# Optimization experiments

Hardware: AMD Instinct MI355X
Metric: run time of the kernel (lower is better)

The kernel has to match this reference:

```python
import jax, jax.numpy as jnp
import numpy as np
from jax import lax

B, T, CIN, H, W = 2, 6, 1, 256, 256
COUT = 64
L = 13
H2, W2 = H // 2, W // 2


def conv2d(x, w, b, stride=1, pad=0):
    y = lax.conv_general_dilated(x, w, (stride, stride), [(pad, pad), (pad, pad)],
                                 dimension_numbers=('NCHW', 'OIHW', 'NCHW'))
    return y + b[None, :, None, None]


def leaky(x):
    return jnp.where(x >= 0, x, 0.2 * x)


def bilinear_sample(img, sx, sy):
    # img [B,C,H,W]; sx,sy [B,L,H,W] pixel coords; zero padding (grid_sample align_corners=True)
    Bc, C, Hh, Ww = img.shape
    x0 = jnp.floor(sx); y0 = jnp.floor(sy)
    x1 = x0 + 1.0; y1 = y0 + 1.0
    wx1 = sx - x0; wx0 = 1.0 - wx1
    wy1 = sy - y0; wy0 = 1.0 - wy1
    img_flat = img.reshape(Bc, C, Hh * Ww)

    def gather(xi, yi):
        valid = (xi >= 0) & (xi <= Ww - 1) & (yi >= 0) & (yi <= Hh - 1)
        xc = jnp.clip(xi, 0, Ww - 1).astype(jnp.int32)
        yc = jnp.clip(yi, 0, Hh - 1).astype(jnp.int32)
        idx = (yc * Ww + xc).reshape(Bc, 1, -1)
        g = jnp.take_along_axis(img_flat, idx, axis=2).reshape(Bc, C, *xi.shape[1:])
        return g * valid[:, None].astype(img.dtype)  # [B,C,L,H,W]

    return (gather(x0, y0) * (wx0 * wy0)[:, None]
            + gather(x1, y0) * (wx1 * wy0)[:, None]
            + gather(x0, y1) * (wx0 * wy1)[:, None]
            + gather(x1, y1) * (wx1 * wy1)[:, None])


def setup_inputs() -> dict:
    key = jax.random.key(0)
    ks = jax.random.split(key, 14)
    s = 0.05
    return {
        'x': jax.random.normal(ks[0], (B, T, CIN, H, W), jnp.float32),
        'w_stem': jax.random.normal(ks[1], (COUT * T, CIN * T, 3, 3), jnp.float32) * s,
        'b_stem': jnp.zeros((COUT * T,), jnp.float32),
        'w_i2h': jax.random.normal(ks[2], (3 * COUT, COUT, 3, 3), jnp.float32) * s,
        'b_i2h': jnp.zeros((3 * COUT,), jnp.float32),
        'w_i2f': jax.random.normal(ks[3], (32, COUT, 5, 5), jnp.float32) * s,
        'b_i2f': jnp.zeros((32,), jnp.float32),
        'w_h2f': jax.random.normal(ks[4], (32, COUT, 5, 5), jnp.float32) * s,
        'b_h2f': jnp.zeros((32,), jnp.float32),
        'w_flow': jax.random.normal(ks[5], (L * 2, 32, 5, 5), jnp.float32) * s,
        'b_flow': jnp.zeros((L * 2,), jnp.float32),
        'w_ret': jax.random.normal(ks[6], (3 * COUT, L * COUT, 1, 1), jnp.float32) * s,
        'b_ret': jnp.zeros((3 * COUT,), jnp.float32),
    }


def reference(x, w_stem, b_stem, w_i2h, b_i2h, w_i2f, b_i2f, w_h2f, b_h2f,
              w_flow, b_flow, w_ret, b_ret):
    Bq, Tq, Cq, Hq, Wq = x.shape
    h2, w2 = Hq // 2, Wq // 2
    # stem: fold T into channels, strided conv + leaky relu
    xs = x.reshape(Bq, Tq * Cq, Hq, Wq)
    ys = leaky(conv2d(xs, w_stem, b_stem, stride=2, pad=1))
    ys = ys.reshape(Bq, Tq, COUT, h2, w2)
    seq = jnp.transpose(ys, (1, 0, 2, 3, 4))  # [T,B,C,h,w]

    gy, gx = jnp.meshgrid(jnp.arange(h2, dtype=jnp.float32),
                          jnp.arange(w2, dtype=jnp.float32), indexing='ij')

    def step(hprev, xt):
        i2h = conv2d(xt, w_i2h, b_i2h, pad=1)  # [B,3C,h,w]
        f1 = leaky(conv2d(xt, w_i2f, b_i2f, pad=2) + conv2d(hprev, w_h2f, b_h2f, pad=2))
        flows = conv2d(f1, w_flow, b_flow, pad=2).reshape(Bq, L, 2, h2, w2)
        u, v = flows[:, :, 0], flows[:, :, 1]
        # wrap(h, -flow): sample at grid - flow
        sx = gx[None, None] - u
        sy = gy[None, None] - v
        warped = bilinear_sample(hprev, sx, sy)  # [B,C,L,h,w]
        warped = jnp.transpose(warped, (0, 2, 1, 3, 4)).reshape(Bq, L * COUT, h2, w2)
        h2h = conv2d(warped, w_ret, b_ret)  # 1x1 conv
        ir, iu, im = jnp.split(i2h, 3, axis=1)
        hr, hu, hm = jnp.split(h2h, 3, axis=1)
        r = jax.nn.sigmoid(ir + hr)
        z = jax.nn.sigmoid(iu + hu)
        m = leaky(im + r * hm)
        hnext = z * hprev + (1.0 - z) * m
        return hnext, hnext

    h0 = jnp.zeros((Bq, COUT, h2, w2), x.dtype)
    _, outs = lax.scan(step, h0, seq)  # [T,B,C,h,w]
    return jnp.transpose(outs, (1, 0, 2, 3, 4))
```

## Files before the change

kernel.cpp:

```cpp
#include <hip/hip_runtime.h>
#include <cstddef>

#define NPIX 16384
#define T_ 6

typedef __attribute__((ext_vector_type(8))) short bf16x8;
typedef __attribute__((ext_vector_type(4))) short bf16x4;
typedef __attribute__((ext_vector_type(4))) float f32x4;
typedef __attribute__((ext_vector_type(4))) unsigned u32x4;
typedef __attribute__((ext_vector_type(2))) unsigned u32x2;

__device__ __forceinline__ float leakyf(float x){ return x >= 0.f ? x : 0.2f*x; }
__device__ __forceinline__ float sigmf(float x){ return 1.f/(1.f+__expf(-x)); }
__device__ __forceinline__ short f2bf(float f){
    unsigned u = __float_as_uint(f);
    u += 0x7fffu + ((u>>16)&1u);
    return (short)(u>>16);
}
__device__ __forceinline__ float bf2f(short s){
    return __uint_as_float(((unsigned)(unsigned short)s)<<16);
}
__device__ __forceinline__ unsigned cvtpk(float lo, float hi){
    unsigned d;
    asm("v_cvt_pk_bf16_f32 %0, %1, %2" : "=v"(d) : "v"(lo), "v"(hi));
    return d;
}
__device__ __forceinline__ f32x4 MFMA(bf16x8 a, bf16x8 b, f32x4 c){
    return __builtin_amdgcn_mfma_f32_16x16x32_bf16(a, b, c, 0, 0, 0);
}
__device__ __forceinline__ void bar_lds(){
    asm volatile("s_waitcnt lgkmcnt(0)" ::: "memory");
    __builtin_amdgcn_s_barrier();
}

__global__ __launch_bounds__(256) void prep_w(const float* __restrict__ wi2h,
        const float* __restrict__ wf1i, const float* __restrict__ wf1h,
        const float* __restrict__ wfl, const float* __restrict__ wrt,
        const float* __restrict__ wst, short* __restrict__ dst){
    int idx = blockIdx.x*256 + threadIdx.x;
    float v;
    if(idx < 110592){
        int kk = idx/12288, r = idx%12288, oc = r>>6, ic = r&63;
        v = wi2h[((size_t)(oc*64+ic))*9 + kk];
    } else if(idx < 212992){
        int j = idx-110592; int tap = j>>11, r = j&2047, oc = r>>6, ic = r&63;
        int inp = tap/25, q = tap%25;
        const float* s = inp ? wf1h : wf1i;
        v = s[((size_t)(oc*64+ic))*25 + q];
    } else if(idx < 238592){
        int j = idx-212992; int q = j>>10, r = j&1023, oc = r>>5, ic = r&31;
        v = (oc < 26) ? wfl[((size_t)(oc*32+ic))*25 + q] : 0.f;
    } else if(idx < 398336){
        int j = idx-238592; int s_ = j/6144, r = j%6144, oc = r>>5, c = r&31;
        v = wrt[(size_t)oc*832 + s_*32 + c];
    } else {
        int j = idx-398336; int oc = j>>6, k = j&63;
        if(k < 54){ int ic = k/9, kk = k%9; v = wst[((size_t)(oc*6+ic))*9 + kk]; }
        else v = 0.f;
    }
    dst[idx] = f2bf(v);
}

__global__ __launch_bounds__(256) void stem_mfma(const float* __restrict__ x,
        const short* __restrict__ wS, const float* __restrict__ bias, short* __restrict__ ys_cl){
    __shared__ float xh[6*17*18];
    int bx = blockIdx.x;
    int ohalf = bx & 1, tile = (bx>>1) & 255, b = bx>>9;
    int ty0 = (tile>>4)*8, tx0 = (tile&15)*8;
    int tid = threadIdx.x, wid = tid>>6, lane = tid&63, lr = lane&15, lg = lane>>4;
    int iy0 = ty0*2-1, ix0 = tx0*2-1;
    for(int i=tid; i<1734; i+=256){
        int ic = i/289, r = i%289, hy = r/17, hx = r%17;
        int iy = iy0+hy, ix = ix0+hx;
        float v = 0.f;
        if((unsigned)iy<256u && (unsigned)ix<256u) v = x[((size_t)b*6+ic)*65536 + iy*256 + ix];
        xh[(ic*17+hy)*18+hx] = v;
    }
    __syncthreads();
    int pxl = wid*16 + lr;
    int ry = (pxl>>3)*2, rx = (pxl&7)*2;
    bf16x8 a[2];
    #pragma unroll
    for(int cg=0; cg<2; ++cg){
        #pragma unroll
        for(int e=0; e<8; ++e){
            int k = cg*32 + lg*8 + e;
            float v = 0.f;
            if(k < 54){
                int ic = k/9, t9 = k%9, ky = t9/3, kx = t9%3;
                v = xh[(ic*17 + ry+ky)*18 + rx+kx];
            }
            a[cg][e] = f2bf(v);
        }
    }
    short* yb = ys_cl + (size_t)b*NPIX*384;
    #pragma unroll
    for(int nj=0; nj<12; ++nj){
        int oc = (ohalf*12 + nj)*16 + lr;
        f32x4 acc = {};
        #pragma unroll
        for(int cg=0; cg<2; ++cg){
            bf16x8 bb = *(const bf16x8*)&wS[(size_t)oc*64 + cg*32 + lg*8];
            acc = MFMA(a[cg], bb, acc);
        }
        float bvs = bias[oc];
        #pragma unroll
        for(int r=0; r<4; ++r){
            int pxr = wid*16 + lg*4 + r;
            int pix = (ty0 + (pxr>>3))*128 + tx0 + (pxr&7);
            yb[(size_t)pix*384 + oc] = f2bf(leakyf(acc[r]+bvs));
        }
    }
}

__global__ __launch_bounds__(512) void ih_if_mfma(const short* __restrict__ ys_cl,
        const short* __restrict__ wI, const float* __restrict__ bI,
        const short* __restrict__ wF,
        short* __restrict__ i2h_all, float* __restrict__ f1i_all){
    __shared__ short xt[432*64];
    int bx = blockIdx.x;
    int tile = bx & 63; int r_ = bx >> 6; int t = r_ % 6; int b = r_ / 6;
    int ty0 = (tile>>2)*8, tx0 = (tile&3)*32;
    int tid = threadIdx.x, wid = tid>>6, lane = tid&63, lr = lane&15, lg = lane>>4;
    int mw = wid>>2, nw = wid&3;
    const short* xb = ys_cl + (size_t)b*NPIX*384 + t*64;
    for(int i=tid; i<3456; i+=512){
        int pix = i>>3, c8 = i&7;
        int hy = pix/36, hx = pix - hy*36;
        int py = ty0 - 2 + hy, px = tx0 - 2 + hx;
        bf16x8 v = {};
        if((unsigned)py < 128u && (unsigned)px < 128u)
            v = *(const bf16x8*)&xb[((size_t)py*128 + px)*384 + c8*8];
        *(bf16x8*)&xt[pix*64 + ((c8 ^ (pix&7))<<3)] = v;
    }
    __syncthreads();
    f32x4 accI[4][2][3] = {};
    for(int kk=0; kk<9; ++kk){
        int ky = kk/3, kx = kk - ky*3;
        #pragma unroll
        for(int cg=0; cg<2; ++cg){
            int ch = cg*4 + lg;
            bf16x8 bv[3];
            #pragma unroll
            for(int ni=0; ni<3; ++ni)
                bv[ni] = *(const bf16x8*)&wI[((size_t)kk*192 + nw*48 + ni*16 + lr)*64 + cg*32 + lg*8];
            #pragma unroll
            for(int ri=0; ri<4; ++ri){
                int r2 = mw*4 + ri;
                bf16x8 av[2];
                #pragma unroll
                for(int mi=0; mi<2; ++mi){
                    int hp = (r2 + ky + 1)*36 + mi*16 + lr + kx + 1;
                    av[mi] = *(const bf16x8*)&xt[hp*64 + ((ch ^ (hp&7))<<3)];
                }
                #pragma unroll
                for(int mi=0; mi<2; ++mi)
                  #pragma unroll
                  for(int ni=0; ni<3; ++ni)
                    accI[ri][mi][ni] = MFMA(av[mi], bv[ni], accI[ri][mi][ni]);
            }
        }
    }
    short* oI = i2h_all + ((size_t)t*2 + b)*192*NPIX;
    #pragma unroll
    for(int ri=0; ri<4; ++ri){
        int py = ty0 + mw*4 + ri;
        #pragma unroll
        for(int mi=0; mi<2; ++mi){
            int px = tx0 + mi*16 + lg*4;
            #pragma unroll
            for(int ni=0; ni<3; ++ni){
                int oc = nw*48 + ni*16 + lr;
                float bvs = bI[oc];
                f32x4 r = accI[ri][mi][ni];
                u32x2 st;
                st[0] = cvtpk(r[0]+bvs, r[1]+bvs);
                st[1] = cvtpk(r[2]+bvs, r[3]+bvs);
                *(u32x2*)&oI[(size_t)oc*NPIX + py*128 + px] = st;
            }
        }
    }
    f32x4 accF[4] = {};
    int mif = nw>>1, jF = (nw&1)*16 + lr;
    for(int q=0; q<25; ++q){
        int ky = q/5, kx = q - ky*5;
        #pragma unroll
        for(int cg=0; cg<2; ++cg){
            int ch = cg*4 + lg;
            bf16x8 bb = *(const bf16x8*)&wF[((size_t)q*32 + (nw&1)*16 + lr)*64 + cg*32 + lg*8];
            #pragma unroll
            for(int ri=0; ri<4; ++ri){
                int hp = (mw*4 + ri + ky)*36 + mif*16 + lr + kx;
                bf16x8 av = *(const bf16x8*)&xt[hp*64 + ((ch ^ (hp&7))<<3)];
                accF[ri] = MFMA(av, bb, accF[ri]);
            }
        }
    }
    float* oF = f1i_all + ((size_t)t*2 + b)*32*NPIX;
    #pragma unroll
    for(int ri=0; ri<4; ++ri){
        int py = ty0 + mw*4 + ri;
        int px = tx0 + mif*16 + lg*4;
        *(f32x4*)&oF[(size_t)jF*NPIX + py*128 + px] = accF[ri];
    }
}

__global__ __launch_bounds__(256) void f1h_mfma(const short* __restrict__ h_cl,
        const short* __restrict__ wF, const float* __restrict__ f1i_all, int t,
        const float* __restrict__ bi, const float* __restrict__ bh,
        short* __restrict__ f1_cl){
    __shared__ short xt[144*64];
    int bx = blockIdx.x;
    int tile = bx & 255, b = bx>>8;
    int ty0 = (tile>>4)*8, tx0 = (tile&15)*8;
    int tid = threadIdx.x, wid = tid>>6, lane = tid&63, lr = lane&15, lg = lane>>4;
    int mw = wid>>1, nw = wid&1;
    const short* xb = h_cl + (size_t)b*NPIX*64;
    for(int i=tid; i<1152; i+=256){
        int pix = i>>3, c8 = i&7;
        int hy = pix/12, hx = pix - hy*12;
        int py = ty0 - 2 + hy, px = tx0 - 2 + hx;
        bf16x8 v = {};
        if((unsigned)py < 128u && (unsigned)px < 128u)
            v = *(const bf16x8*)&xb[((size_t)py*128 + px)*64 + c8*8];
        *(bf16x8*)&xt[pix*64 + ((c8 ^ (pix&7))<<3)] = v;
    }
    __syncthreads();
    f32x4 acc[2] = {};
    for(int q=0; q<25; ++q){
        int ky = q/5, kx = q - ky*5;
        #pragma unroll
        for(int cg=0; cg<2; ++cg){
            int ch = cg*4 + lg;
            bf16x8 av[2];
            #pragma unroll
            for(int mi=0; mi<2; ++mi){
                int m = mw*32 + mi*16 + lr;
                int hp = ((m>>3)+ky)*12 + (m&7)+kx;
                av[mi] = *(const bf16x8*)&xt[hp*64 + ((ch ^ (hp&7))<<3)];
            }
            bf16x8 bb = *(const bf16x8*)&wF[((size_t)(25+q)*32 + nw*16 + lr)*64 + cg*32 + lg*8];
            #pragma unroll
            for(int mi=0; mi<2; ++mi) acc[mi] = MFMA(av[mi], bb, acc[mi]);
        }
    }
    int j = nw*16 + lr;
    float bvs = bi[j] + bh[j];
    const float* pF = f1i_all + ((size_t)t*2 + b)*32*NPIX;
    __syncthreads();
    #pragma unroll
    for(int mi=0; mi<2; ++mi){
        int m0 = mw*32 + mi*16 + lg*4;
        int py = ty0 + (m0>>3), px = tx0 + (m0&7);
        f32x4 p = *(const f32x4*)&pF[(size_t)j*NPIX + py*128 + px];
        #pragma unroll
        for(int r=0; r<4; ++r) xt[(m0+r)*40 + j] = f2bf(leakyf(acc[mi][r] + p[r] + bvs));
    }
    __syncthreads();
    {
        int px = tid>>2, c8 = tid&3;
        int pix = (ty0 + (px>>3))*128 + tx0 + (px&7);
        *(bf16x8*)&f1_cl[((size_t)b*NPIX + pix)*32 + c8*8] = *(const bf16x8*)&xt[px*40 + c8*8];
    }
}

__global__ __launch_bounds__(256) void flow_mfma(const short* __restrict__ f1_cl,
        const short* __restrict__ wA, const float* __restrict__ bias, float* __restrict__ flows){
    __shared__ short xt[144*40];
    int bx = blockIdx.x;
    int tile = bx & 255, b = bx>>8;
    int ty0 = (tile>>4)*8, tx0 = (tile&15)*8;
    int tid = threadIdx.x, wid = tid>>6, lane = tid&63, lr = lane&15, lg = lane>>4;
    int mw = wid>>1, nw = wid&1;
    f32x4 acc[2] = {};
    const short* xb = f1_cl + (size_t)b*NPIX*32;
    for(int i=tid; i<576; i+=256){
        int pix = i>>2, c8 = i&3;
        int hy = pix/12, hx = pix - hy*12;
        int py = ty0 - 2 + hy, px = tx0 - 2 + hx;
        bf16x8 v = {};
        if((unsigned)py < 128u && (unsigned)px < 128u)
            v = *(const bf16x8*)&xb[((size_t)py*128 + px)*32 + c8*8];
        *(bf16x8*)&xt[pix*40 + c8*8] = v;
    }
    __syncthreads();
    for(int ky=0; ky<5; ++ky){
        #pragma unroll
        for(int kx=0; kx<5; ++kx){
            bf16x8 av[2];
            #pragma unroll
            for(int mi=0; mi<2; ++mi){
                int m = mw*32 + mi*16 + lr;
                int hp = ((m>>3)+ky)*12 + (m&7) + kx;
                av[mi] = *(const bf16x8*)&xt[hp*40 + lg*8];
            }
            bf16x8 bb = *(const bf16x8*)&wA[((size_t)((ky*5+kx)*32) + nw*16 + lr)*32 + lg*8];
            #pragma unroll
            for(int mi=0; mi<2; ++mi) acc[mi] = MFMA(av[mi], bb, acc[mi]);
        }
    }
    int j = nw*16 + lr;
    if(j < 26){
        float bvs = bias[j];
        #pragma unroll
        for(int mi=0; mi<2; ++mi){
            int m0 = mw*32 + mi*16 + lg*4;
            int py = ty0 + (m0>>3), px = tx0 + (m0&7);
            f32x4 r = acc[mi];
            f32x4 st; st[0]=r[0]+bvs; st[1]=r[1]+bvs; st[2]=r[2]+bvs; st[3]=r[3]+bvs;
            *(f32x4*)&flows[((size_t)b*26 + j)*NPIX + py*128 + px] = st;
        }
    }
}

__device__ __forceinline__ void calc_corners(const float* __restrict__ s_sx,
        const float* __restrict__ s_sy, int l, int mypx,
        int& i00, int& i10, int& i01, int& i11,
        float& w00, float& w10, float& w01, float& w11){
    float sx = s_sx[l*64+mypx], sy = s_sy[l*64+mypx];
    float x0f = floorf(sx), y0f = floorf(sy);
    int x0 = (int)x0f, y0 = (int)y0f;
    float wx1 = sx-x0f, wy1 = sy-y0f, wx0 = 1.f-wx1, wy0 = 1.f-wy1;
    bool vx0 = (unsigned)x0<128u, vx1 = (unsigned)(x0+1)<128u;
    bool vy0 = (unsigned)y0<128u, vy1 = (unsigned)(y0+1)<128u;
    w00 = (vx0&&vy0)? wx0*wy0 : 0.f;
    w10 = (vx1&&vy0)? wx1*wy0 : 0.f;
    w01 = (vx0&&vy1)? wx0*wy1 : 0.f;
    w11 = (vx1&&vy1)? wx1*wy1 : 0.f;
    int xc0 = max(0,min(127,x0)), xc1 = max(0,min(127,x0+1));
    int yc0 = max(0,min(127,y0)), yc1 = max(0,min(127,y0+1));
    i00 = yc0*128+xc0; i10 = yc0*128+xc1; i01 = yc1*128+xc0; i11 = yc1*128+xc1;
}

__global__ __launch_bounds__(256) void warpret_mfma(
        const float* __restrict__ hprev_f32, int hstride,
        const short* __restrict__ h_in,
        const float* __restrict__ flows,
        const short* __restrict__ wret, const float* __restrict__ b_ret,
        const short* __restrict__ ib_bf, float* __restrict__ out,
        short* __restrict__ h_out, int t){
    __shared__ float s_sx[832], s_sy[832];
    __shared__ short At[2][64*32];
    __shared__ short Bt[2][192*32];
    int bx = blockIdx.x;
    int half = bx & 1, row = (bx>>1) & 127, b = bx >> 8;
    int pxbase = half*64;
    int tid = threadIdx.x, wid = tid>>6, lane = tid&63, lr = lane&15, lg = lane>>4;
    const short* hc = h_in + (size_t)b*NPIX*64;
    f32x4 acc[12] = {};
    for(int i=tid; i<832; i+=256){
        int l = i>>6, px = i&63;
        float u = flows[((size_t)b*26 + 2*l)*NPIX + row*128 + pxbase + px];
        float v = flows[((size_t)b*26 + 2*l+1)*NPIX + row*128 + pxbase + px];
        s_sx[i] = (float)(pxbase+px) - u;
        s_sy[i] = (float)row - v;
    }
    __syncthreads();

    int spx = tid & 63, sch = tid >> 6;
    int brow = tid >> 2, bc4 = tid & 3;
    int aslot = (sch ^ ((spx>>1)&3))<<3;
    int bslot = (bc4 ^ ((brow>>1)&3))<<3;
    int rslot = (lg ^ ((lr>>1)&3))<<3;

    auto issue = [&](int sp, bf16x8& g00, bf16x8& g10, bf16x8& g01, bf16x8& g11,
                     bf16x8& q0, bf16x8& q1, bf16x8& q2,
                     float& w00, float& w10, float& w01, float& w11){
        int i00,i10,i01,i11;
        calc_corners(s_sx, s_sy, sp>>1, spx, i00,i10,i01,i11, w00,w10,w01,w11);
        int cb = (sp&1)*32 + sch*8;
        g00 = *(const bf16x8*)&hc[(size_t)i00*64 + cb];
        g10 = *(const bf16x8*)&hc[(size_t)i10*64 + cb];
        g01 = *(const bf16x8*)&hc[(size_t)i01*64 + cb];
        g11 = *(const bf16x8*)&hc[(size_t)i11*64 + cb];
        q0 = *(const bf16x8*)&wret[((size_t)sp*192 + brow      )*32 + bc4*8];
        q1 = *(const bf16x8*)&wret[((size_t)sp*192 + brow +  64)*32 + bc4*8];
        q2 = *(const bf16x8*)&wret[((size_t)sp*192 + brow + 128)*32 + bc4*8];
    };
    auto commit = [&](int buf, bf16x8 g00, bf16x8 g10, bf16x8 g01, bf16x8 g11,
                      bf16x8 q0, bf16x8 q1, bf16x8 q2,
                      float w00, float w10, float w01, float w11){
        float r[8];
        #pragma unroll
        for(int e=0; e<8; ++e)
            r[e] = bf2f(g00[e])*w00 + bf2f(g10[e])*w10 +
                   bf2f(g01[e])*w01 + bf2f(g11[e])*w11;
        u32x4 av;
        av[0] = cvtpk(r[0], r[1]);
        av[1] = cvtpk(r[2], r[3]);
        av[2] = cvtpk(r[4], r[5]);
        av[3] = cvtpk(r[6], r[7]);
        *(u32x4*)&At[buf][spx*32 + aslot] = av;
        *(bf16x8*)&Bt[buf][(brow      )*32 + bslot] = q0;
        *(bf16x8*)&Bt[buf][(brow +  64)*32 + bslot] = q1;
        *(bf16x8*)&Bt[buf][(brow + 128)*32 + bslot] = q2;
    };

    {
        bf16x8 g00,g10,g01,g11,q0,q1,q2; float w00,w10,w01,w11;
        issue(0, g00,g10,g01,g11,q0,q1,q2, w00,w10,w01,w11);
        commit(0, g00,g10,g01,g11,q0,q1,q2, w00,w10,w01,w11);
    }
    bf16x8 p00,p10,p01,p11,pq0,pq1,pq2; float v00,v10,v01,v11;
    issue(1, p00,p10,p01,p11,pq0,pq1,pq2, v00,v10,v01,v11);
    bar_lds();

    for(int s=0; s<26; ++s){
        int cur = s & 1, nxt = cur ^ 1;
        bf16x8 n00,n10,n01,n11,nq0,nq1,nq2; float u00,u10,u01,u11;
        if(s < 24)
            issue(s+2, n00,n10,n01,n11,nq0,nq1,nq2, u00,u10,u01,u11);
        {
            bf16x8 a = *(const bf16x8*)&At[cur][(wid*16 + lr)*32 + rslot];
            #pragma unroll
            for(int ni=0; ni<12; ++ni){
                bf16x8 bb = *(const bf16x8*)&Bt[cur][(ni*16 + lr)*32 + rslot];
                acc[ni] = MFMA(a, bb, acc[ni]);
            }
        }
        if(s < 25)
            commit(nxt, p00,p10,p01,p11,pq0,pq1,pq2, v00,v10,v01,v11);
        bar_lds();
        if(s < 24){
            p00=n00; p10=n10; p01=n01; p11=n11;
            pq0=nq0; pq1=nq1; pq2=nq2;
            v00=u00; v10=u10; v01=u01; v11=u11;
        }
    }

    short* Ht = &Bt[0][0];
    const short* ib = ib_bf + (size_t)b*192*NPIX + row*128 + pxbase;
    const float* hbf = hprev_f32 + (size_t)b*hstride + row*128 + pxbase;
    float* ob = out + (((size_t)b*T_ + t)*64)*NPIX + row*128 + pxbase;
    int px4 = wid*16 + lg*4;
    #pragma unroll
    for(int ni=0; ni<4; ++ni){
        int oc = ni*16 + lr;
        bf16x4 irv = *(const bf16x4*)&ib[(size_t)oc*NPIX + px4];
        bf16x4 iuv = *(const bf16x4*)&ib[(size_t)(64+oc)*NPIX + px4];
        bf16x4 imv = *(const bf16x4*)&ib[(size_t)(128+oc)*NPIX + px4];
        f32x4 hp = *(const f32x4*)&hbf[(size_t)oc*NPIX + px4];
        float br = b_ret[oc], bu = b_ret[64+oc], bm = b_ret[128+oc];
        f32x4 st;
        #pragma unroll
        for(int r=0; r<4; ++r){
            float hr = acc[ni][r] + br;
            float hu = acc[ni+4][r] + bu;
            float hm = acc[ni+8][r] + bm;
            float rg = sigmf(bf2f(irv[r]) + hr);
            float zg = sigmf(bf2f(iuv[r]) + hu);
            float mg = leakyf(bf2f(imv[r]) + rg*hm);
            st[r] = zg*hp[r] + (1.f-zg)*mg;
        }
        *(f32x4*)&ob[(size_t)oc*NPIX + px4] = st;
        #pragma unroll
        for(int r=0; r<4; ++r) Ht[(px4+r)*72 + oc] = f2bf(st[r]);
    }
    __syncthreads();
    short* ho = h_out + ((size_t)b*NPIX + row*128 + pxbase)*64;
    for(int i=tid; i<512; i+=256){
        int px = i>>3, c8 = i&7;
        *(bf16x8*)&ho[(size_t)px*64 + c8*8] = *(const bf16x8*)&Ht[px*72 + c8*8];
    }
}

extern "C" void kernel_launch(void* const* d_in, const int* in_sizes, int n_in,
                              void* d_out, int out_size, void* d_ws, size_t ws_size,
                              hipStream_t stream) {
    const float* x      = (const float*)d_in[0];
    const float* w_stem = (const float*)d_in[1];
    const float* b_stem = (const float*)d_in[2];
    const float* w_i2h  = (const float*)d_in[3];
    const float* b_i2h  = (const float*)d_in[4];
    const float* w_i2f  = (const float*)d_in[5];
    const float* b_i2f  = (const float*)d_in[6];
    const float* w_h2f  = (const float*)d_in[7];
    const float* b_h2f  = (const float*)d_in[8];
    const float* w_flow = (const float*)d_in[9];
    const float* b_flow = (const float*)d_in[10];
    const float* w_ret  = (const float*)d_in[11];
    const float* b_ret  = (const float*)d_in[12];
    float* out = (float*)d_out;

    char* w = (char*)d_ws;
    float* h0_f32  = (float*)w;  w += (size_t)2*64*NPIX*4;
    short* i2h_all = (short*)w;  w += (size_t)6*2*192*NPIX*2;
    float* f1i_all = (float*)w;  w += (size_t)6*2*32*NPIX*4;
    float* flows   = (float*)w;  w += (size_t)2*26*NPIX*4;
    short* ys_cl   = (short*)w;  w += (size_t)2*NPIX*384*2;
    short* h_clA   = (short*)w;  w += (size_t)2*NPIX*64*2;
    short* h_clB   = (short*)w;  w += (size_t)2*NPIX*64*2;
    short* f1_cl   = (short*)w;  w += (size_t)2*NPIX*32*2;
    short* wAbase  = (short*)w;
    short* wA_i2h  = wAbase;
    short* wA_f1   = wAbase + 110592;
    short* wA_flow = wAbase + 212992;
    short* wA_ret  = wAbase + 238592;
    short* wA_stem = wAbase + 398336;

    prep_w<<<1652, 256, 0, stream>>>(w_i2h, w_i2f, w_h2f, w_flow, w_ret, w_stem, wAbase);
    hipMemsetAsync(h0_f32, 0, (size_t)2*64*NPIX*4, stream);
    hipMemsetAsync(h_clA, 0, (size_t)2*NPIX*64*2, stream);

    stem_mfma<<<1024, 256, 0, stream>>>(x, wA_stem, b_stem, ys_cl);
    ih_if_mfma<<<768, 512, 0, stream>>>(ys_cl, wA_i2h, b_i2h, wA_f1, i2h_all, f1i_all);

    for (int t = 0; t < T_; ++t) {
        const float* hprev = (t == 0) ? h0_f32 : out + (size_t)(t - 1) * 64 * NPIX;
        int hstride = (t == 0) ? 64 * NPIX : T_ * 64 * NPIX;
        short* h_in  = (t & 1) ? h_clB : h_clA;
        short* h_nxt = (t & 1) ? h_clA : h_clB;
        f1h_mfma<<<512, 256, 0, stream>>>(h_in, wA_f1, f1i_all, t, b_i2f, b_h2f, f1_cl);
        flow_mfma<<<512, 256, 0, stream>>>(f1_cl, wA_flow, b_flow, flows);
        warpret_mfma<<<512, 256, 0, stream>>>(hprev, hstride, h_in, flows,
                                              wA_ret, b_ret,
                                              i2h_all + (size_t)t*2*192*NPIX,
                                              out, h_nxt, t);
    }
}
```

Before: 501.4 us.

## Retile i2h conv warps and load warp-return weights directly to registers

In the i2h/i2f conv kernel, the 8 waves are regrouped as 4x2 instead of 2x4. Each wave now covers 2 rows by 96 output channels, which raises B-fragment reuse per A load and cuts redundant LDS reads. In warpret, the 1x1 return-conv weights are no longer staged through double-buffered LDS. Each wave reads its MFMA B fragments straight from global memory each step, and the gather prefetch depth drops from two stages to one. This saves LDS space and stores, at the cost of more global/L2 weight traffic per wave and less latency hiding for the bilinear gathers.

```diff
diff --git a/kernel.cpp b/kernel.cpp
--- a/kernel.cpp
+++ b/kernel.cpp
@@ -122,7 +122,7 @@
     int tile = bx & 63; int r_ = bx >> 6; int t = r_ % 6; int b = r_ / 6;
     int ty0 = (tile>>2)*8, tx0 = (tile&3)*32;
     int tid = threadIdx.x, wid = tid>>6, lane = tid&63, lr = lane&15, lg = lane>>4;
-    int mw = wid>>2, nw = wid&3;
+    int mw = wid>>1, nw = wid&1;
     const short* xb = ys_cl + (size_t)b*NPIX*384 + t*64;
     for(int i=tid; i<3456; i+=512){
         int pix = i>>3, c8 = i&7;
@@ -134,19 +134,19 @@
         *(bf16x8*)&xt[pix*64 + ((c8 ^ (pix&7))<<3)] = v;
     }
     __syncthreads();
-    f32x4 accI[4][2][3] = {};
+    f32x4 accI[2][2][6] = {};
     for(int kk=0; kk<9; ++kk){
         int ky = kk/3, kx = kk - ky*3;
         #pragma unroll
         for(int cg=0; cg<2; ++cg){
             int ch = cg*4 + lg;
-            bf16x8 bv[3];
-            #pragma unroll
-            for(int ni=0; ni<3; ++ni)
-                bv[ni] = *(const bf16x8*)&wI[((size_t)kk*192 + nw*48 + ni*16 + lr)*64 + cg*32 + lg*8];
-            #pragma unroll
-            for(int ri=0; ri<4; ++ri){
-                int r2 = mw*4 + ri;
+            bf16x8 bv[6];
+            #pragma unroll
+            for(int ni=0; ni<6; ++ni)
+                bv[ni] = *(const bf16x8*)&wI[((size_t)kk*192 + nw*96 + ni*16 + lr)*64 + cg*32 + lg*8];
+            #pragma unroll
+            for(int ri=0; ri<2; ++ri){
+                int r2 = mw*2 + ri;
                 bf16x8 av[2];
                 #pragma unroll
                 for(int mi=0; mi<2; ++mi){
@@ -156,21 +156,21 @@
                 #pragma unroll
                 for(int mi=0; mi<2; ++mi)
                   #pragma unroll
-                  for(int ni=0; ni<3; ++ni)
+                  for(int ni=0; ni<6; ++ni)
                     accI[ri][mi][ni] = MFMA(av[mi], bv[ni], accI[ri][mi][ni]);
             }
         }
     }
     short* oI = i2h_all + ((size_t)t*2 + b)*192*NPIX;
     #pragma unroll
-    for(int ri=0; ri<4; ++ri){
-        int py = ty0 + mw*4 + ri;
+    for(int ri=0; ri<2; ++ri){
+        int py = ty0 + mw*2 + ri;
         #pragma unroll
         for(int mi=0; mi<2; ++mi){
             int px = tx0 + mi*16 + lg*4;
             #pragma unroll
-            for(int ni=0; ni<3; ++ni){
-                int oc = nw*48 + ni*16 + lr;
+            for(int ni=0; ni<6; ++ni){
+                int oc = nw*96 + ni*16 + lr;
                 float bvs = bI[oc];
                 f32x4 r = accI[ri][mi][ni];
                 u32x2 st;
@@ -180,28 +180,34 @@
             }
         }
     }
-    f32x4 accF[4] = {};
-    int mif = nw>>1, jF = (nw&1)*16 + lr;
+    f32x4 accF[2][2] = {};
+    int jF = nw*16 + lr;
     for(int q=0; q<25; ++q){
         int ky = q/5, kx = q - ky*5;
         #pragma unroll
         for(int cg=0; cg<2; ++cg){
             int ch = cg*4 + lg;
-            bf16x8 bb = *(const bf16x8*)&wF[((size_t)q*32 + (nw&1)*16 + lr)*64 + cg*32 + lg*8];
-            #pragma unroll
-            for(int ri=0; ri<4; ++ri){
-                int hp = (mw*4 + ri + ky)*36 + mif*16 + lr + kx;
-                bf16x8 av = *(const bf16x8*)&xt[hp*64 + ((ch ^ (hp&7))<<3)];
-                accF[ri] = MFMA(av, bb, accF[ri]);
+            bf16x8 bb = *(const bf16x8*)&wF[((size_t)q*32 + nw*16 + lr)*64 + cg*32 + lg*8];
+            #pragma unroll
+            for(int ri=0; ri<2; ++ri){
+                #pragma unroll
+                for(int mi=0; mi<2; ++mi){
+                    int hp = (mw*2 + ri + ky)*36 + mi*16 + lr + kx;
+                    bf16x8 av = *(const bf16x8*)&xt[hp*64 + ((ch ^ (hp&7))<<3)];
+                    accF[ri][mi] = MFMA(av, bb, accF[ri][mi]);
+                }
             }
         }
     }
     float* oF = f1i_all + ((size_t)t*2 + b)*32*NPIX;
     #pragma unroll
-    for(int ri=0; ri<4; ++ri){
-        int py = ty0 + mw*4 + ri;
-        int px = tx0 + mif*16 + lg*4;
-        *(f32x4*)&oF[(size_t)jF*NPIX + py*128 + px] = accF[ri];
+    for(int ri=0; ri<2; ++ri){
+        int py = ty0 + mw*2 + ri;
+        #pragma unroll
+        for(int mi=0; mi<2; ++mi){
+            int px = tx0 + mi*16 + lg*4;
+            *(f32x4*)&oF[(size_t)jF*NPIX + py*128 + px] = accF[ri][mi];
+        }
     }
 }
 
@@ -341,7 +347,7 @@
         short* __restrict__ h_out, int t){
     __shared__ float s_sx[832], s_sy[832];
     __shared__ short At[2][64*32];
-    __shared__ short Bt[2][192*32];
+    __shared__ short Ht[64*72];
     int bx = blockIdx.x;
     int half = bx & 1, row = (bx>>1) & 127, b = bx >> 8;
     int pxbase = half*64;
@@ -358,14 +364,11 @@
     __syncthreads();
 
     int spx = tid & 63, sch = tid >> 6;
-    int brow = tid >> 2, bc4 = tid & 3;
     int aslot = (sch ^ ((spx>>1)&3))<<3;
-    int bslot = (bc4 ^ ((brow>>1)&3))<<3;
     int rslot = (lg ^ ((lr>>1)&3))<<3;
 
-    auto issue = [&](int sp, bf16x8& g00, bf16x8& g10, bf16x8& g01, bf16x8& g11,
-                     bf16x8& q0, bf16x8& q1, bf16x8& q2,
-                     float& w00, float& w10, float& w01, float& w11){
+    auto issueA = [&](int sp, bf16x8& g00, bf16x8& g10, bf16x8& g01, bf16x8& g11,
+                      float& w00, float& w10, float& w01, float& w11){
         int i00,i10,i01,i11;
         calc_corners(s_sx, s_sy, sp>>1, spx, i00,i10,i01,i11, w00,w10,w01,w11);
         int cb = (sp&1)*32 + sch*8;
@@ -373,13 +376,9 @@
         g10 = *(const bf16x8*)&hc[(size_t)i10*64 + cb];
         g01 = *(const bf16x8*)&hc[(size_t)i01*64 + cb];
         g11 = *(const bf16x8*)&hc[(size_t)i11*64 + cb];
-        q0 = *(const bf16x8*)&wret[((size_t)sp*192 + brow      )*32 + bc4*8];
-        q1 = *(const bf16x8*)&wret[((size_t)sp*192 + brow +  64)*32 + bc4*8];
-        q2 = *(const bf16x8*)&wret[((size_t)sp*192 + brow + 128)*32 + bc4*8];
     };
-    auto commit = [&](int buf, bf16x8 g00, bf16x8 g10, bf16x8 g01, bf16x8 g11,
-                      bf16x8 q0, bf16x8 q1, bf16x8 q2,
-                      float w00, float w10, float w01, float w11){
+    auto commitA = [&](int buf, bf16x8 g00, bf16x8 g10, bf16x8 g01, bf16x8 g11,
+                       float w00, float w10, float w01, float w11){
         float r[8];
         #pragma unroll
         for(int e=0; e<8; ++e)
@@ -391,44 +390,35 @@
         av[2] = cvtpk(r[4], r[5]);
         av[3] = cvtpk(r[6], r[7]);
         *(u32x4*)&At[buf][spx*32 + aslot] = av;
-        *(bf16x8*)&Bt[buf][(brow      )*32 + bslot] = q0;
-        *(bf16x8*)&Bt[buf][(brow +  64)*32 + bslot] = q1;
-        *(bf16x8*)&Bt[buf][(brow + 128)*32 + bslot] = q2;
     };
 
     {
-        bf16x8 g00,g10,g01,g11,q0,q1,q2; float w00,w10,w01,w11;
-        issue(0, g00,g10,g01,g11,q0,q1,q2, w00,w10,w01,w11);
-        commit(0, g00,g10,g01,g11,q0,q1,q2, w00,w10,w01,w11);
-    }
-    bf16x8 p00,p10,p01,p11,pq0,pq1,pq2; float v00,v10,v01,v11;
-    issue(1, p00,p10,p01,p11,pq0,pq1,pq2, v00,v10,v01,v11);
+        bf16x8 g00,g10,g01,g11; float w00,w10,w01,w11;
+        issueA(0, g00,g10,g01,g11, w00,w10,w01,w11);
+        commitA(0, g00,g10,g01,g11, w00,w10,w01,w11);
+    }
     bar_lds();
 
     for(int s=0; s<26; ++s){
         int cur = s & 1, nxt = cur ^ 1;
-        bf16x8 n00,n10,n01,n11,nq0,nq1,nq2; float u00,u10,u01,u11;
-        if(s < 24)
-            issue(s+2, n00,n10,n01,n11,nq0,nq1,nq2, u00,u10,u01,u11);
+        bf16x8 Bv[12];
+        #pragma unroll
+        for(int ni=0; ni<12; ++ni)
+            Bv[ni] = *(const bf16x8*)&wret[((size_t)s*192 + ni*16 + lr)*32 + lg*8];
+        bf16x8 p00,p10,p01,p11; float v00=0,v10=0,v01=0,v11=0;
+        if(s < 25)
+            issueA(s+1, p00,p10,p01,p11, v00,v10,v01,v11);
         {
             bf16x8 a = *(const bf16x8*)&At[cur][(wid*16 + lr)*32 + rslot];
             #pragma unroll
-            for(int ni=0; ni<12; ++ni){
-                bf16x8 bb = *(const bf16x8*)&Bt[cur][(ni*16 + lr)*32 + rslot];
-                acc[ni] = MFMA(a, bb, acc[ni]);
-            }
+            for(int ni=0; ni<12; ++ni)
+                acc[ni] = MFMA(a, Bv[ni], acc[ni]);
         }
         if(s < 25)
-            commit(nxt, p00,p10,p01,p11,pq0,pq1,pq2, v00,v10,v01,v11);
+            commitA(nxt, p00,p10,p01,p11, v00,v10,v01,v11);
         bar_lds();
-        if(s < 24){
-            p00=n00; p10=n10; p01=n01; p11=n11;
-            pq0=nq0; pq1=nq1; pq2=nq2;
-            v00=u00; v10=u10; v01=u01; v11=u11;
-        }
-    }
-
-    short* Ht = &Bt[0][0];
+    }
+
     const short* ib = ib_bf + (size_t)b*192*NPIX + row*128 + pxbase;
     const float* hbf = hprev_f32 + (size_t)b*hstride + row*128 + pxbase;
     float* ob = out + (((size_t)b*T_ + t)*64)*NPIX + row*128 + pxbase;
```

Result: slower. 705.0 us (+40.6%).
